# Performance work log

Measured on AMD Instinct MI355X. Metric: run time of the kernel, lower is better.

Reference implementation:

```python
import jax, jax.numpy as jnp
import numpy as np

HIDDEN_SIZE = 256
INPUT_SIZE = 4
N_CLASSES = 2
START_VALUE_PADDING = -100.0


def setup_inputs() -> dict:
    key = jax.random.key(0)
    ks = jax.random.split(key, 11)
    B, T = 128, 2048
    H, IN = HIDDEN_SIZE, INPUT_SIZE
    s = 1.0 / np.sqrt(H)  # torch LSTM/Linear default init scale
    u = lambda k, shape: jax.random.uniform(k, shape, jnp.float32, -s, s)
    return {
        "y": jax.random.normal(ks[0], (B, T), dtype=jnp.float32),
        "W_ih0": u(ks[1], (4 * H, IN)),
        "W_hh0": u(ks[2], (4 * H, H)),
        "b_ih0": u(ks[3], (4 * H,)),
        "b_hh0": u(ks[4], (4 * H,)),
        "W_ih1": u(ks[5], (4 * H, H)),
        "W_hh1": u(ks[6], (4 * H, H)),
        "b_ih1": u(ks[7], (4 * H,)),
        "b_hh1": u(ks[8], (4 * H,)),
        "W_fc": u(ks[9], (N_CLASSES, H)),
        "b_fc": u(ks[10], (N_CLASSES,)),
    }


def _cell(x, h, c, W_ih, W_hh, b):
    # torch LSTM gate order: i, f, g, o
    g = x @ W_ih.T + h @ W_hh.T + b
    i, f, gg, o = jnp.split(g, 4, axis=-1)
    c = jax.nn.sigmoid(f) * c + jax.nn.sigmoid(i) * jnp.tanh(gg)
    h = jax.nn.sigmoid(o) * jnp.tanh(c)
    return h, c


def reference(y, W_ih0, W_hh0, b_ih0, b_hh0, W_ih1, W_hh1, b_ih1, b_hh1, W_fc, b_fc):
    B, T = y.shape
    H, IN = HIDDEN_SIZE, INPUT_SIZE
    # torch roll-on-padded-array windowing == prepend IN-1 pad values,
    # window t = [y_pre[t], ..., y_pre[t+IN-1]] (oldest-first, current sample last)
    y_pre = jnp.concatenate(
        [jnp.full((B, IN - 1), START_VALUE_PADDING, y.dtype), y], axis=1)
    idx = jnp.arange(T)[:, None] + jnp.arange(IN)[None, :]  # [T, IN]
    seq = y_pre[:, idx]  # [B, T, IN]

    b0 = b_ih0 + b_hh0
    b1 = b_ih1 + b_hh1

    def step(carry, x_t):
        h1, c1, h2, c2 = carry
        h1, c1 = _cell(x_t, h1, c1, W_ih0, W_hh0, b0)
        h2, c2 = _cell(h1, h2, c2, W_ih1, W_hh1, b1)
        return (h1, c1, h2, c2), h2

    z = jnp.zeros((B, H), y.dtype)
    _, hs = jax.lax.scan(step, (z, z, z, z), seq.transpose(1, 0, 2))  # hs: [T,B,H]
    lstm_out = hs.transpose(1, 0, 2)  # [B, T, H]
    out = lstm_out @ W_fc.T + b_fc  # [B, T, N_CLASSES]  (phase='train')
    return out
```

## Files before the change

### kernel.cpp

```cpp
#include <hip/hip_runtime.h>
#include <math.h>

#define T_LEN 2048
#define NGRP  16
#define NSLC  16
#define BPG   8
#define NTH   512

typedef __attribute__((ext_vector_type(8))) short short8v;
typedef __attribute__((ext_vector_type(4))) float f32x4;
typedef unsigned int u32t;
typedef unsigned long long u64t;

#define H1G_OFF 0
#define H2G_OFF 65536
#define FLG_OFF 131072
#define ABT_OFF (131072 + 512)
#define WS_U32  (131072 + 512 + 1)

#define L_H1HI 0
#define L_H1LO 8448
#define L_H2HI 16896
#define L_H2LO 25344
#define HROWB  528

__device__ __forceinline__ float sigm(float x) { return 1.0f / (1.0f + expf(-x)); }

__device__ __forceinline__ u32t bf_rn(float x) {
  u32t b; __builtin_memcpy(&b, &x, 4);
  return (b + 0x7FFFu + ((b >> 16) & 1u)) >> 16;
}
__device__ __forceinline__ void split_bf(float x, u32t& hi, u32t& lo) {
  hi = bf_rn(x);
  u32t hb = hi << 16; float hf; __builtin_memcpy(&hf, &hb, 4);
  lo = bf_rn(x - hf);
}

__global__ void init_ws_kernel(u32t* ws) {
  for (int i = blockIdx.x * blockDim.x + threadIdx.x; i < WS_U32;
       i += gridDim.x * blockDim.x)
    ws[i] = 0;
}

__launch_bounds__(NTH, 2)
__global__ void lstm_persist(const float* __restrict__ y,
                             const float* __restrict__ Wih0, const float* __restrict__ Whh0,
                             const float* __restrict__ bih0, const float* __restrict__ bhh0,
                             const float* __restrict__ Wih1, const float* __restrict__ Whh1,
                             const float* __restrict__ bih1, const float* __restrict__ bhh1,
                             const float* __restrict__ Wfc, const float* __restrict__ bfc,
                             float* __restrict__ out, u32t* wsu) {
  extern __shared__ char lds[];
  const int tid   = threadIdx.x;
  const int lane  = tid & 63;
  const int wid   = tid >> 6;
  const int group = blockIdx.x & 15;
  const int slice = blockIdx.x >> 4;

  u32t* flags  = wsu + FLG_OFF + group * 32;
  u32t* abortf = wsu + ABT_OFF;

  for (int i = tid; i < 1056; i += NTH) {
    ((u32t*)(lds + L_H1HI))[1056 + i] = 0;
    ((u32t*)(lds + L_H1LO))[1056 + i] = 0;
    ((u32t*)(lds + L_H2HI))[1056 + i] = 0;
    ((u32t*)(lds + L_H2LO))[1056 + i] = 0;
  }

  const int m     = lane & 15;
  const int kq4   = lane >> 4;
  const int gateA = m & 3, hs4A = m >> 2;
  const int hidA  = slice * 16 + (wid & 3) * 4 + hs4A;
  const int growA = gateA * 256 + hidA;

  const bool isL1  = (wid >= 4);
  const bool hasFC = (wid == 0 && slice == 0);
  const float* WA = isL1 ? Wih1 : Whh0;
  const float* WB = isL1 ? Whh1 : Wfc;
  const int   rowB  = isL1 ? growA : m;
  const bool  bValid = isL1 || (hasFC && m < 2);

  short8v ahi[16], alo[16];
  #pragma unroll
  for (int ks = 0; ks < 8; ++ks) {
    short8v h0, l0, h1, l1;
    #pragma unroll
    for (int j = 0; j < 8; ++j) {
      int k = ks * 32 + kq4 * 8 + j;
      u32t hi, lo;
      split_bf(WA[growA * 256 + k], hi, lo);
      h0[j] = (short)hi; l0[j] = (short)lo;
      float vb = bValid ? WB[rowB * 256 + k] : 0.f;
      split_bf(vb, hi, lo);
      h1[j] = (short)hi; l1[j] = (short)lo;
    }
    ahi[ks] = h0;     alo[ks] = l0;
    ahi[8 + ks] = h1; alo[8 + ks] = l1;
  }

  const int batch = lane & 15;
  const int hidC  = slice * 16 + (wid & 3) * 4 + (lane >> 4);
  float bias4[4], wx[16];
  #pragma unroll
  for (int r = 0; r < 4; ++r) {
    int row = r * 256 + hidC;
    bias4[r] = isL1 ? (bih1[row] + bhh1[row]) : (bih0[row] + bhh0[row]);
    #pragma unroll
    for (int kk = 0; kk < 4; ++kk)
      wx[r * 4 + kk] = isL1 ? 0.f : Wih0[row * 4 + kk];
  }
  float bfc0 = 0.f, bfc1 = 0.f;
  if (hasFC) { bfc0 = bfc[0]; bfc1 = bfc[1]; }
  const float* yb = y + (group * BPG + (batch & 7)) * T_LEN;

  float cst = 0.f;

  __syncthreads();

  for (int p = 0; p <= T_LEN + 1; ++p) {
    const bool doL0 = !isL1 && (p < T_LEN);
    const bool doL1 = isL1 && (p >= 1 && p <= T_LEN);
    const bool doFC = hasFC && (p >= 2);

    {
      const u64t* s1 = (const u64t*)(wsu + H1G_OFF + ((p & 1) ^ 1) * 32768 + group * 2048);
      const u64t* s2 = (const u64t*)(wsu + H2G_OFF + (p & 1) * 32768 + group * 2048);
      #pragma unroll
      for (int it = 0; it < 2; ++it) {
        int idx = tid + it * NTH;
        int ba  = (idx >> 7) * HROWB + (idx & 127) * 4;
        u64t v1 = __hip_atomic_load(s1 + idx, __ATOMIC_RELAXED, __HIP_MEMORY_SCOPE_AGENT);
        u64t v2 = __hip_atomic_load(s2 + idx, __ATOMIC_RELAXED, __HIP_MEMORY_SCOPE_AGENT);
        u32t a0 = (u32t)v1, a1 = (u32t)(v1 >> 32);
        *(u32t*)(lds + L_H1HI + ba) = (a0 >> 16) | (a1 & 0xFFFF0000u);
        *(u32t*)(lds + L_H1LO + ba) = (a0 & 0xFFFFu) | (a1 << 16);
        u32t b0 = (u32t)v2, b1 = (u32t)(v2 >> 32);
        *(u32t*)(lds + L_H2HI + ba) = (b0 >> 16) | (b1 & 0xFFFF0000u);
        *(u32t*)(lds + L_H2LO + ba) = (b0 & 0xFFFFu) | (b1 << 16);
      }
    }
    __syncthreads();

    f32x4 acc = {0.f, 0.f, 0.f, 0.f}, accF = {0.f, 0.f, 0.f, 0.f};
    const int bfoff = (lane & 15) * HROWB + (lane >> 4) * 16;
    if (doL0) {
      #pragma unroll
      for (int ks = 0; ks < 8; ++ks) {
        short8v bh = *(const short8v*)(lds + L_H1HI + bfoff + ks * 64);
        short8v bl = *(const short8v*)(lds + L_H1LO + bfoff + ks * 64);
        acc = __builtin_amdgcn_mfma_f32_16x16x32_bf16(ahi[ks], bh, acc, 0, 0, 0);
        acc = __builtin_amdgcn_mfma_f32_16x16x32_bf16(ahi[ks], bl, acc, 0, 0, 0);
        acc = __builtin_amdgcn_mfma_f32_16x16x32_bf16(alo[ks], bh, acc, 0, 0, 0);
      }
    }
    if (doL1) {
      #pragma unroll
      for (int ks = 0; ks < 8; ++ks) {
        short8v b1h = *(const short8v*)(lds + L_H1HI + bfoff + ks * 64);
        short8v b1l = *(const short8v*)(lds + L_H1LO + bfoff + ks * 64);
        short8v b2h = *(const short8v*)(lds + L_H2HI + bfoff + ks * 64);
        short8v b2l = *(const short8v*)(lds + L_H2LO + bfoff + ks * 64);
        acc = __builtin_amdgcn_mfma_f32_16x16x32_bf16(ahi[ks], b1h, acc, 0, 0, 0);
        acc = __builtin_amdgcn_mfma_f32_16x16x32_bf16(ahi[ks], b1l, acc, 0, 0, 0);
        acc = __builtin_amdgcn_mfma_f32_16x16x32_bf16(alo[ks], b1h, acc, 0, 0, 0);
        acc = __builtin_amdgcn_mfma_f32_16x16x32_bf16(ahi[8 + ks], b2h, acc, 0, 0, 0);
        acc = __builtin_amdgcn_mfma_f32_16x16x32_bf16(ahi[8 + ks], b2l, acc, 0, 0, 0);
        acc = __builtin_amdgcn_mfma_f32_16x16x32_bf16(alo[8 + ks], b2h, acc, 0, 0, 0);
      }
    }
    if (doFC) {
      #pragma unroll
      for (int ks = 0; ks < 8; ++ks) {
        short8v b2h = *(const short8v*)(lds + L_H2HI + bfoff + ks * 64);
        short8v b2l = *(const short8v*)(lds + L_H2LO + bfoff + ks * 64);
        accF = __builtin_amdgcn_mfma_f32_16x16x32_bf16(ahi[8 + ks], b2h, accF, 0, 0, 0);
        accF = __builtin_amdgcn_mfma_f32_16x16x32_bf16(ahi[8 + ks], b2l, accF, 0, 0, 0);
        accF = __builtin_amdgcn_mfma_f32_16x16x32_bf16(alo[8 + ks], b2h, accF, 0, 0, 0);
      }
    }

    if (doL0 || doL1) {
      float g[4];
      #pragma unroll
      for (int r = 0; r < 4; ++r) g[r] = acc[r] + bias4[r];
      if (doL0) {
        #pragma unroll
        for (int kk = 0; kk < 4; ++kk) {
          int ti = p + kk - 3;
          float xv = (ti >= 0) ? yb[ti] : -100.0f;
          #pragma unroll
          for (int r = 0; r < 4; ++r) g[r] = fmaf(wx[r * 4 + kk], xv, g[r]);
        }
      }
      cst = sigm(g[1]) * cst + sigm(g[0]) * tanhf(g[2]);
      float hv = sigm(g[3]) * tanhf(cst);
      u32t hi, lo; split_bf(hv, hi, lo);
      u32t pk = (hi << 16) | lo;
      if (batch < BPG) {
        u32t* dst = isL1
            ? (wsu + H2G_OFF + ((p & 1) ^ 1) * 32768 + group * 2048 + batch * 256 + hidC)
            : (wsu + H1G_OFF + (p & 1) * 32768 + group * 2048 + batch * 256 + hidC);
        __hip_atomic_store(dst, pk, __ATOMIC_RELAXED, __HIP_MEMORY_SCOPE_AGENT);
      }
    }
    if (doFC && lane < 8) {
      out[(group * BPG + lane) * (T_LEN * 2) + (p - 2) * 2 + 0] = accF[0] + bfc0;
      out[(group * BPG + lane) * (T_LEN * 2) + (p - 2) * 2 + 1] = accF[1] + bfc1;
    }

    if (p == T_LEN + 1) break;

    asm volatile("s_waitcnt vmcnt(0)" ::: "memory");
    __syncthreads();
    if (tid == 0)
      __hip_atomic_store(&flags[slice], (u32t)(p + 1),
                         __ATOMIC_RELAXED, __HIP_MEMORY_SCOPE_AGENT);
    {
      const u32t tgt = (u32t)(p + 1);
      bool ok = false;
      for (int it = 0; it < (1 << 20); ++it) {
        u32t f = __hip_atomic_load(&flags[lane & 15],
                                   __ATOMIC_RELAXED, __HIP_MEMORY_SCOPE_AGENT);
        if (__all(f >= tgt)) { ok = true; break; }
        if ((it & 63) == 63 &&
            __hip_atomic_load(abortf, __ATOMIC_RELAXED, __HIP_MEMORY_SCOPE_AGENT) != 0)
          break;
        __builtin_amdgcn_s_sleep(1);
      }
      if (!ok) __hip_atomic_store(abortf, 1, __ATOMIC_RELAXED, __HIP_MEMORY_SCOPE_AGENT);
    }
  }
}

extern "C" void kernel_launch(void* const* d_in, const int* in_sizes, int n_in,
                              void* d_out, int out_size, void* d_ws, size_t ws_size,
                              hipStream_t stream) {
  const float* y    = (const float*)d_in[0];
  const float* Wih0 = (const float*)d_in[1];
  const float* Whh0 = (const float*)d_in[2];
  const float* bih0 = (const float*)d_in[3];
  const float* bhh0 = (const float*)d_in[4];
  const float* Wih1 = (const float*)d_in[5];
  const float* Whh1 = (const float*)d_in[6];
  const float* bih1 = (const float*)d_in[7];
  const float* bhh1 = (const float*)d_in[8];
  const float* Wfc  = (const float*)d_in[9];
  const float* bfc  = (const float*)d_in[10];
  float* out = (float*)d_out;
  u32t* ws   = (u32t*)d_ws;

  (void)hipFuncSetAttribute(reinterpret_cast<const void*>(lstm_persist),
                            hipFuncAttributeMaxDynamicSharedMemorySize, 131072);

  hipLaunchKernelGGL(init_ws_kernel, dim3(64), dim3(256), 0, stream, ws);
  hipLaunchKernelGGL(lstm_persist, dim3(256), dim3(NTH), 131072, stream,
                     y, Wih0, Whh0, bih0, bhh0, Wih1, Whh1, bih1, bhh1,
                     Wfc, bfc, out, ws);
}
```

Before: 6.621 ms.

## Replace flag barrier with tagged per-element data sync and split-K waves

Replaces the per-step flag-based barrier across the blocks of a group with 64-bit hidden-state entries that carry a timestep tag. Consumers spin on the tags of exactly the data they need, and the buffers become four-deep rings. The partitioning also changes to 8 groups of 16 batches with 32 slices of 8 hidden units. The K dimension is split across wave pairs, which combine their partial sums through LDS, and the staging LDS gets an XOR swizzle and double buffering. This is meant to remove the global barrier round-trip and its sleep latency from each recurrent step, at the cost of doubled global traffic for the tags, an extra intra-block sync, and more polling loads.

After: 26.20 ms. +295.8%, slower.

```diff
diff --git a/kernel.cpp b/kernel.cpp
--- a/kernel.cpp
+++ b/kernel.cpp
@@ -2,9 +2,9 @@
 #include <math.h>
 
 #define T_LEN 2048
-#define NGRP  16
-#define NSLC  16
-#define BPG   8
+#define NGRP  8
+#define NSLC  32
+#define BPG   16
 #define NTH   512
 
 typedef __attribute__((ext_vector_type(8))) short short8v;
@@ -12,17 +12,14 @@
 typedef unsigned int u32t;
 typedef unsigned long long u64t;
 
-#define H1G_OFF 0
-#define H2G_OFF 65536
-#define FLG_OFF 131072
-#define ABT_OFF (131072 + 512)
-#define WS_U32  (131072 + 512 + 1)
-
-#define L_H1HI 0
-#define L_H1LO 8448
-#define L_H2HI 16896
-#define L_H2LO 25344
-#define HROWB  528
+#define H1_OFF  0
+#define H2_OFF  131072
+#define ABT_OFF 262144
+#define WS_U64  262145
+
+#define STG_SZ   65536
+#define PART_OFF 65536
+#define FCP_OFF  69632
 
 __device__ __forceinline__ float sigm(float x) { return 1.0f / (1.0f + expf(-x)); }
 
@@ -36,11 +33,13 @@
   lo = bf_rn(x - hf);
 }
 
-__global__ void init_ws_kernel(u32t* ws) {
-  for (int i = blockIdx.x * blockDim.x + threadIdx.x; i < WS_U32;
+__global__ void init_ws_kernel(u64t* ws) {
+  for (int i = blockIdx.x * blockDim.x + threadIdx.x; i < WS_U64;
        i += gridDim.x * blockDim.x)
-    ws[i] = 0;
-}
+    ws[i] = 0ull;
+}
+
+#define MFMA16(a, b, c) __builtin_amdgcn_mfma_f32_16x16x32_bf16(a, b, c, 0, 0, 0)
 
 __launch_bounds__(NTH, 2)
 __global__ void lstm_persist(const float* __restrict__ y,
@@ -49,185 +48,260 @@
                              const float* __restrict__ Wih1, const float* __restrict__ Whh1,
                              const float* __restrict__ bih1, const float* __restrict__ bhh1,
                              const float* __restrict__ Wfc, const float* __restrict__ bfc,
-                             float* __restrict__ out, u32t* wsu) {
+                             float* __restrict__ out, u64t* wsu) {
   extern __shared__ char lds[];
   const int tid   = threadIdx.x;
   const int lane  = tid & 63;
   const int wid   = tid >> 6;
-  const int group = blockIdx.x & 15;
-  const int slice = blockIdx.x >> 4;
-
-  u32t* flags  = wsu + FLG_OFF + group * 32;
-  u32t* abortf = wsu + ABT_OFF;
-
-  for (int i = tid; i < 1056; i += NTH) {
-    ((u32t*)(lds + L_H1HI))[1056 + i] = 0;
-    ((u32t*)(lds + L_H1LO))[1056 + i] = 0;
-    ((u32t*)(lds + L_H2HI))[1056 + i] = 0;
-    ((u32t*)(lds + L_H2LO))[1056 + i] = 0;
+  const int group = blockIdx.x & 7;
+  const int slice = blockIdx.x >> 3;
+
+  u64t* h1b    = wsu + H1_OFF;
+  u64t* h2b    = wsu + H2_OFF;
+  u64t* abortf = wsu + ABT_OFF;
+
+  for (int i = tid; i < STG_SZ / 4; i += NTH) ((u32t*)lds)[i] = 0;
+
+  const bool isL1 = (wid >= 4);
+  const int  tl   = (wid & 3) >> 1;
+  const int  kh   = wid & 1;
+  const int  hidb = slice * 8 + tl * 4;
+
+  const int m = lane & 15, kq4 = lane >> 4;
+  const int gateA = m & 3, hs4A = m >> 2;
+  const int growA = gateA * 256 + hidb + hs4A;
+
+  short8v ahi[8], alo[8];
+  if (!isL1) {
+    const int ksb = kh * 4;
+    #pragma unroll
+    for (int ksl = 0; ksl < 4; ++ksl) {
+      short8v h8, l8;
+      #pragma unroll
+      for (int j = 0; j < 8; ++j) {
+        int k = (ksb + ksl) * 32 + kq4 * 8 + j;
+        u32t hi, lo; split_bf(Whh0[growA * 256 + k], hi, lo);
+        h8[j] = (short)hi; l8[j] = (short)lo;
+      }
+      ahi[ksl] = h8; alo[ksl] = l8;
+    }
+  } else {
+    const float* WA = kh ? Whh1 : Wih1;
+    #pragma unroll
+    for (int ksl = 0; ksl < 8; ++ksl) {
+      short8v h8, l8;
+      #pragma unroll
+      for (int j = 0; j < 8; ++j) {
+        int k = ksl * 32 + kq4 * 8 + j;
+        u32t hi, lo; split_bf(WA[growA * 256 + k], hi, lo);
+        h8[j] = (short)hi; l8[j] = (short)lo;
+      }
+      ahi[ksl] = h8; alo[ksl] = l8;
+    }
   }
 
-  const int m     = lane & 15;
-  const int kq4   = lane >> 4;
-  const int gateA = m & 3, hs4A = m >> 2;
-  const int hidA  = slice * 16 + (wid & 3) * 4 + hs4A;
-  const int growA = gateA * 256 + hidA;
-
-  const bool isL1  = (wid >= 4);
-  const bool hasFC = (wid == 0 && slice == 0);
-  const float* WA = isL1 ? Wih1 : Whh0;
-  const float* WB = isL1 ? Whh1 : Wfc;
-  const int   rowB  = isL1 ? growA : m;
-  const bool  bValid = isL1 || (hasFC && m < 2);
-
-  short8v ahi[16], alo[16];
-  #pragma unroll
-  for (int ks = 0; ks < 8; ++ks) {
-    short8v h0, l0, h1, l1;
-    #pragma unroll
-    for (int j = 0; j < 8; ++j) {
-      int k = ks * 32 + kq4 * 8 + j;
-      u32t hi, lo;
-      split_bf(WA[growA * 256 + k], hi, lo);
-      h0[j] = (short)hi; l0[j] = (short)lo;
-      float vb = bValid ? WB[rowB * 256 + k] : 0.f;
-      split_bf(vb, hi, lo);
-      h1[j] = (short)hi; l1[j] = (short)lo;
-    }
-    ahi[ks] = h0;     alo[ks] = l0;
-    ahi[8 + ks] = h1; alo[8 + ks] = l1;
+  const bool fcw  = (slice == 0) && (wid == 1 || wid == 3);
+  const int  fksb = (wid == 3) ? 4 : 0;
+  short8v fhi[4], flo[4];
+  if (fcw) {
+    #pragma unroll
+    for (int ksl = 0; ksl < 4; ++ksl) {
+      short8v h8, l8;
+      #pragma unroll
+      for (int j = 0; j < 8; ++j) {
+        int k = (fksb + ksl) * 32 + kq4 * 8 + j;
+        float w = (m < 2) ? Wfc[m * 256 + k] : 0.f;
+        u32t hi, lo; split_bf(w, hi, lo);
+        h8[j] = (short)hi; l8[j] = (short)lo;
+      }
+      fhi[ksl] = h8; flo[ksl] = l8;
+    }
   }
 
-  const int batch = lane & 15;
-  const int hidC  = slice * 16 + (wid & 3) * 4 + (lane >> 4);
-  float bias4[4], wx[16];
-  #pragma unroll
-  for (int r = 0; r < 4; ++r) {
-    int row = r * 256 + hidC;
-    bias4[r] = isL1 ? (bih1[row] + bhh1[row]) : (bih0[row] + bhh0[row]);
-    #pragma unroll
-    for (int kk = 0; kk < 4; ++kk)
-      wx[r * 4 + kk] = isL1 ? 0.f : Wih0[row * 4 + kk];
+  const int hidC = hidb + kq4;
+  float bias4[4] = {0, 0, 0, 0}, wx4[16];
+  if (wid == 0 || wid == 2) {
+    #pragma unroll
+    for (int r = 0; r < 4; ++r) {
+      int row = r * 256 + hidC;
+      bias4[r] = bih0[row] + bhh0[row];
+      #pragma unroll
+      for (int kk = 0; kk < 4; ++kk) wx4[r * 4 + kk] = Wih0[row * 4 + kk];
+    }
+  } else if (wid == 4 || wid == 6) {
+    #pragma unroll
+    for (int r = 0; r < 4; ++r) {
+      int row = r * 256 + hidC;
+      bias4[r] = bih1[row] + bhh1[row];
+    }
   }
   float bfc0 = 0.f, bfc1 = 0.f;
-  if (hasFC) { bfc0 = bfc[0]; bfc1 = bfc[1]; }
-  const float* yb = y + (group * BPG + (batch & 7)) * T_LEN;
+  if (slice == 0 && wid == 3) { bfc0 = bfc[0]; bfc1 = bfc[1]; }
+  const float* yb = y + (group * BPG + m) * T_LEN;
 
   float cst = 0.f;
 
+  const int srow = tid >> 5;
+  const int k0e  = (tid & 31) * 8;
+  const int sxr  = (srow & 7) << 4;
+  const int scb  = (tid & 31) * 16;
+
   __syncthreads();
 
   for (int p = 0; p <= T_LEN + 1; ++p) {
-    const bool doL0 = !isL1 && (p < T_LEN);
-    const bool doL1 = isL1 && (p >= 1 && p <= T_LEN);
-    const bool doFC = hasFC && (p >= 2);
-
+    const int  pp    = p & 1;
+    const bool need1 = (p >= 1 && p <= T_LEN);
+    const bool need2 = (p >= 2 && p <= T_LEN + 1);
+
+    u64t v1[8], v2[8];
     {
-      const u64t* s1 = (const u64t*)(wsu + H1G_OFF + ((p & 1) ^ 1) * 32768 + group * 2048);
-      const u64t* s2 = (const u64t*)(wsu + H2G_OFF + (p & 1) * 32768 + group * 2048);
-      #pragma unroll
-      for (int it = 0; it < 2; ++it) {
-        int idx = tid + it * NTH;
-        int ba  = (idx >> 7) * HROWB + (idx & 127) * 4;
-        u64t v1 = __hip_atomic_load(s1 + idx, __ATOMIC_RELAXED, __HIP_MEMORY_SCOPE_AGENT);
-        u64t v2 = __hip_atomic_load(s2 + idx, __ATOMIC_RELAXED, __HIP_MEMORY_SCOPE_AGENT);
-        u32t a0 = (u32t)v1, a1 = (u32t)(v1 >> 32);
-        *(u32t*)(lds + L_H1HI + ba) = (a0 >> 16) | (a1 & 0xFFFF0000u);
-        *(u32t*)(lds + L_H1LO + ba) = (a0 & 0xFFFFu) | (a1 << 16);
-        u32t b0 = (u32t)v2, b1 = (u32t)(v2 >> 32);
-        *(u32t*)(lds + L_H2HI + ba) = (b0 >> 16) | (b1 & 0xFFFF0000u);
-        *(u32t*)(lds + L_H2LO + ba) = (b0 & 0xFFFFu) | (b1 << 16);
+      const u64t* s1 = h1b + (u64t)((p - 1) & 3) * 32768 + group * 4096 + srow * 256 + k0e;
+      const u64t* s2 = h2b + (u64t)((p - 2) & 3) * 32768 + group * 4096 + srow * 256 + k0e;
+      const u32t tg1 = (u32t)(p + 15), tg2 = (u32t)(p + 14);
+      u32t st1 = need1 ? 0xFFu : 0u, st2 = need2 ? 0xFFu : 0u;
+      int guard = 0;
+      while (st1 | st2) {
+        #pragma unroll
+        for (int j = 0; j < 8; ++j)
+          if (st1 & (1u << j))
+            v1[j] = __hip_atomic_load(s1 + j, __ATOMIC_RELAXED, __HIP_MEMORY_SCOPE_AGENT);
+        #pragma unroll
+        for (int j = 0; j < 8; ++j)
+          if (st2 & (1u << j))
+            v2[j] = __hip_atomic_load(s2 + j, __ATOMIC_RELAXED, __HIP_MEMORY_SCOPE_AGENT);
+        u32t n1 = 0, n2 = 0;
+        #pragma unroll
+        for (int j = 0; j < 8; ++j)
+          if ((st1 & (1u << j)) && (u32t)(v1[j] >> 32) != tg1) n1 |= 1u << j;
+        #pragma unroll
+        for (int j = 0; j < 8; ++j)
+          if ((st2 & (1u << j)) && (u32t)(v2[j] >> 32) != tg2) n2 |= 1u << j;
+        st1 = n1; st2 = n2;
+        if (st1 | st2) {
+          ++guard;
+          if (guard > (1 << 16)) {
+            __hip_atomic_store(abortf, 1ull, __ATOMIC_RELAXED, __HIP_MEMORY_SCOPE_AGENT);
+            break;
+          }
+          if ((guard & 63) == 0 &&
+              __hip_atomic_load(abortf, __ATOMIC_RELAXED, __HIP_MEMORY_SCOPE_AGENT) != 0)
+            break;
+        }
+      }
+    }
+
+    float xx[4];
+    if ((wid == 0 || wid == 2) && p < T_LEN) {
+      #pragma unroll
+      for (int kk = 0; kk < 4; ++kk) {
+        int ti = p + kk - 3;
+        xx[kk] = (ti >= 0) ? yb[ti] : -100.0f;
+      }
+    }
+
+    {
+      char* base = lds + pp * 32768;
+      if (need1) {
+        short8v vh, vl;
+        #pragma unroll
+        for (int j = 0; j < 8; ++j) {
+          u32t pk = (u32t)v1[j];
+          vh[j] = (short)(pk >> 16); vl[j] = (short)(pk & 0xFFFFu);
+        }
+        *(short8v*)(base + srow * 512 + (scb ^ sxr))        = vh;
+        *(short8v*)(base + 8192 + srow * 512 + (scb ^ sxr)) = vl;
+      }
+      if (need2) {
+        short8v vh, vl;
+        #pragma unroll
+        for (int j = 0; j < 8; ++j) {
+          u32t pk = (u32t)v2[j];
+          vh[j] = (short)(pk >> 16); vl[j] = (short)(pk & 0xFFFFu);
+        }
+        *(short8v*)(base + 16384 + srow * 512 + (scb ^ sxr)) = vh;
+        *(short8v*)(base + 24576 + srow * 512 + (scb ^ sxr)) = vl;
       }
     }
     __syncthreads();
 
-    f32x4 acc = {0.f, 0.f, 0.f, 0.f}, accF = {0.f, 0.f, 0.f, 0.f};
-    const int bfoff = (lane & 15) * HROWB + (lane >> 4) * 16;
-    if (doL0) {
-      #pragma unroll
-      for (int ks = 0; ks < 8; ++ks) {
-        short8v bh = *(const short8v*)(lds + L_H1HI + bfoff + ks * 64);
-        short8v bl = *(const short8v*)(lds + L_H1LO + bfoff + ks * 64);
-        acc = __builtin_amdgcn_mfma_f32_16x16x32_bf16(ahi[ks], bh, acc, 0, 0, 0);
-        acc = __builtin_amdgcn_mfma_f32_16x16x32_bf16(ahi[ks], bl, acc, 0, 0, 0);
-        acc = __builtin_amdgcn_mfma_f32_16x16x32_bf16(alo[ks], bh, acc, 0, 0, 0);
-      }
-    }
-    if (doL1) {
-      #pragma unroll
-      for (int ks = 0; ks < 8; ++ks) {
-        short8v b1h = *(const short8v*)(lds + L_H1HI + bfoff + ks * 64);
-        short8v b1l = *(const short8v*)(lds + L_H1LO + bfoff + ks * 64);
-        short8v b2h = *(const short8v*)(lds + L_H2HI + bfoff + ks * 64);
-        short8v b2l = *(const short8v*)(lds + L_H2LO + bfoff + ks * 64);
-        acc = __builtin_amdgcn_mfma_f32_16x16x32_bf16(ahi[ks], b1h, acc, 0, 0, 0);
-        acc = __builtin_amdgcn_mfma_f32_16x16x32_bf16(ahi[ks], b1l, acc, 0, 0, 0);
-        acc = __builtin_amdgcn_mfma_f32_16x16x32_bf16(alo[ks], b1h, acc, 0, 0, 0);
-        acc = __builtin_amdgcn_mfma_f32_16x16x32_bf16(ahi[8 + ks], b2h, acc, 0, 0, 0);
-        acc = __builtin_amdgcn_mfma_f32_16x16x32_bf16(ahi[8 + ks], b2l, acc, 0, 0, 0);
-        acc = __builtin_amdgcn_mfma_f32_16x16x32_bf16(alo[8 + ks], b2h, acc, 0, 0, 0);
-      }
-    }
-    if (doFC) {
-      #pragma unroll
-      for (int ks = 0; ks < 8; ++ks) {
-        short8v b2h = *(const short8v*)(lds + L_H2HI + bfoff + ks * 64);
-        short8v b2l = *(const short8v*)(lds + L_H2LO + bfoff + ks * 64);
-        accF = __builtin_amdgcn_mfma_f32_16x16x32_bf16(ahi[8 + ks], b2h, accF, 0, 0, 0);
-        accF = __builtin_amdgcn_mfma_f32_16x16x32_bf16(ahi[8 + ks], b2l, accF, 0, 0, 0);
-        accF = __builtin_amdgcn_mfma_f32_16x16x32_bf16(alo[8 + ks], b2h, accF, 0, 0, 0);
-      }
-    }
-
-    if (doL0 || doL1) {
-      float g[4];
-      #pragma unroll
-      for (int r = 0; r < 4; ++r) g[r] = acc[r] + bias4[r];
-      if (doL0) {
-        #pragma unroll
-        for (int kk = 0; kk < 4; ++kk) {
-          int ti = p + kk - 3;
-          float xv = (ti >= 0) ? yb[ti] : -100.0f;
+    const int brow = lane & 15;
+    const int bxr  = (brow & 7) << 4;
+    const int bco  = (lane >> 4) * 16;
+    char* sb = lds + pp * 32768;
+#define BRD(mat, pl, ks) \
+  (*(const short8v*)(sb + (mat) * 16384 + (pl) * 8192 + brow * 512 + ((((ks) * 64) + bco) ^ bxr)))
+
+    f32x4 acc = {0.f, 0.f, 0.f, 0.f};
+    if (!isL1) {
+      if (p < T_LEN) {
+        const int ksb = kh * 4;
+        #pragma unroll
+        for (int ksl = 0; ksl < 4; ++ksl) {
+          short8v bh = BRD(0, 0, ksb + ksl), bl = BRD(0, 1, ksb + ksl);
+          acc = MFMA16(ahi[ksl], bh, acc);
+          acc = MFMA16(ahi[ksl], bl, acc);
+          acc = MFMA16(alo[ksl], bh, acc);
+        }
+      }
+    } else {
+      if (p >= 1 && p <= T_LEN) {
+        #pragma unroll
+        for (int ksl = 0; ksl < 8; ++ksl) {
+          short8v bh = kh ? BRD(1, 0, ksl) : BRD(0, 0, ksl);
+          short8v bl = kh ? BRD(1, 1, ksl) : BRD(0, 1, ksl);
+          acc = MFMA16(ahi[ksl], bh, acc);
+          acc = MFMA16(ahi[ksl], bl, acc);
+          acc = MFMA16(alo[ksl], bh, acc);
+        }
+      }
+    }
+    f32x4 accF = {0.f, 0.f, 0.f, 0.f};
+    if (fcw && p >= 2) {
+      #pragma unroll
+      for (int ksl = 0; ksl < 4; ++ksl) {
+        short8v bh = BRD(1, 0, fksb + ksl), bl = BRD(1, 1, fksb + ksl);
+        accF = MFMA16(fhi[ksl], bh, accF);
+        accF = MFMA16(fhi[ksl], bl, accF);
+        accF = MFMA16(flo[ksl], bh, accF);
+      }
+    }
+
+    if (wid & 1) *(f32x4*)(lds + PART_OFF + (wid >> 1) * 1024 + lane * 16) = acc;
+    if (fcw && wid == 1) *(f32x4*)(lds + FCP_OFF + lane * 16) = accF;
+    __syncthreads();
+
+    if (!(wid & 1)) {
+      const bool act = isL1 ? (p >= 1 && p <= T_LEN) : (p < T_LEN);
+      if (act) {
+        f32x4 po = *(const f32x4*)(lds + PART_OFF + (wid >> 1) * 1024 + lane * 16);
+        float g[4];
+        #pragma unroll
+        for (int r = 0; r < 4; ++r) g[r] = acc[r] + po[r] + bias4[r];
+        if (!isL1) {
           #pragma unroll
-          for (int r = 0; r < 4; ++r) g[r] = fmaf(wx[r * 4 + kk], xv, g[r]);
-        }
-      }
-      cst = sigm(g[1]) * cst + sigm(g[0]) * tanhf(g[2]);
-      float hv = sigm(g[3]) * tanhf(cst);
-      u32t hi, lo; split_bf(hv, hi, lo);
-      u32t pk = (hi << 16) | lo;
-      if (batch < BPG) {
-        u32t* dst = isL1
-            ? (wsu + H2G_OFF + ((p & 1) ^ 1) * 32768 + group * 2048 + batch * 256 + hidC)
-            : (wsu + H1G_OFF + (p & 1) * 32768 + group * 2048 + batch * 256 + hidC);
+          for (int kk = 0; kk < 4; ++kk)
+            #pragma unroll
+            for (int r = 0; r < 4; ++r) g[r] = fmaf(wx4[r * 4 + kk], xx[kk], g[r]);
+        }
+        cst = sigm(g[1]) * cst + sigm(g[0]) * tanhf(g[2]);
+        float hv = sigm(g[3]) * tanhf(cst);
+        u32t hi, lo; split_bf(hv, hi, lo);
+        const u32t tag = (u32t)(isL1 ? (p + 15) : (p + 16));
+        u64t pk = ((u64t)tag << 32) | (u64t)((hi << 16) | lo);
+        u64t* dst = isL1
+            ? (h2b + (u64t)((p - 1) & 3) * 32768 + group * 4096 + m * 256 + hidC)
+            : (h1b + (u64t)(p & 3) * 32768 + group * 4096 + m * 256 + hidC);
         __hip_atomic_store(dst, pk, __ATOMIC_RELAXED, __HIP_MEMORY_SCOPE_AGENT);
       }
     }
-    if (doFC && lane < 8) {
-      out[(group * BPG + lane) * (T_LEN * 2) + (p - 2) * 2 + 0] = accF[0] + bfc0;
-      out[(group * BPG + lane) * (T_LEN * 2) + (p - 2) * 2 + 1] = accF[1] + bfc1;
-    }
-
-    if (p == T_LEN + 1) break;
-
-    asm volatile("s_waitcnt vmcnt(0)" ::: "memory");
-    __syncthreads();
-    if (tid == 0)
-      __hip_atomic_store(&flags[slice], (u32t)(p + 1),
-                         __ATOMIC_RELAXED, __HIP_MEMORY_SCOPE_AGENT);
-    {
-      const u32t tgt = (u32t)(p + 1);
-      bool ok = false;
-      for (int it = 0; it < (1 << 20); ++it) {
-        u32t f = __hip_atomic_load(&flags[lane & 15],
-                                   __ATOMIC_RELAXED, __HIP_MEMORY_SCOPE_AGENT);
-        if (__all(f >= tgt)) { ok = true; break; }
-        if ((it & 63) == 63 &&
-            __hip_atomic_load(abortf, __ATOMIC_RELAXED, __HIP_MEMORY_SCOPE_AGENT) != 0)
-          break;
-        __builtin_amdgcn_s_sleep(1);
-      }
-      if (!ok) __hip_atomic_store(abortf, 1, __ATOMIC_RELAXED, __HIP_MEMORY_SCOPE_AGENT);
+    if (wid == 3 && slice == 0 && p >= 2) {
+      f32x4 pf = *(const f32x4*)(lds + FCP_OFF + lane * 16);
+      if (lane < 16) {
+        float2 o;
+        o.x = accF[0] + pf[0] + bfc0;
+        o.y = accF[1] + pf[1] + bfc1;
+        *(float2*)(&out[(group * BPG + lane) * (T_LEN * 2) + (p - 2) * 2]) = o;
+      }
     }
   }
 }
@@ -247,13 +321,13 @@
   const float* Wfc  = (const float*)d_in[9];
   const float* bfc  = (const float*)d_in[10];
   float* out = (float*)d_out;
-  u32t* ws   = (u32t*)d_ws;
+  u64t*  ws  = (u64t*)d_ws;
 
   (void)hipFuncSetAttribute(reinterpret_cast<const void*>(lstm_persist),
                             hipFuncAttributeMaxDynamicSharedMemorySize, 131072);
 
-  hipLaunchKernelGGL(init_ws_kernel, dim3(64), dim3(256), 0, stream, ws);
-  hipLaunchKernelGGL(lstm_persist, dim3(256), dim3(NTH), 131072, stream,
+  hipLaunchKernelGGL(init_ws_kernel, dim3(256), dim3(256), 0, stream, ws);
+  hipLaunchKernelGGL(lstm_persist, dim3(NGRP * NSLC), dim3(NTH), 131072, stream,
                      y, Wih0, Whh0, bih0, bhh0, Wih1, Whh1, bih1, bhh1,
                      Wfc, bfc, out, ws);
 }
```
